# Kernel optimization log

Measured on AMD Instinct MI355X. Metric: run time of the kernel, lower is better.

Reference implementation:

```python
import jax, jax.numpy as jnp
import numpy as np
import math

EMBED = 1024
HEADS = 16
B, S = 2, 1024

def setup_inputs() -> dict:
    key = jax.random.key(0)
    ks = jax.random.split(key, 6)
    sc = 1.0 / math.sqrt(EMBED)
    return {
        "x": jax.random.normal(ks[0], (B, S, EMBED), dtype=jnp.float32),
        "Wq": jax.random.normal(ks[1], (EMBED, EMBED), dtype=jnp.float32) * sc,
        "Wk": jax.random.normal(ks[2], (EMBED, EMBED), dtype=jnp.float32) * sc,
        "Wv": jax.random.normal(ks[3], (EMBED, EMBED), dtype=jnp.float32) * sc,
        "Wo": jax.random.normal(ks[4], (EMBED, EMBED), dtype=jnp.float32) * sc,
        "bo": jax.random.normal(ks[5], (EMBED,), dtype=jnp.float32) * sc,
        "heads": HEADS,
    }

def reference(x, Wq, Wk, Wv, Wo, bo, heads):
    nB, nS, nE = x.shape
    nH = heads
    nG = nE // nH  # effective number of 'heads' in this (quirky) module

    def split(W):
        # (B,S,E) -> (B,S,G,H) -> (B,G,S,H); per-head dim is nH (as in source)
        return (x @ W).reshape(nB, nS, nG, nH).transpose(0, 2, 1, 3)

    q, k, v = split(Wq), split(Wk), split(Wv)
    # scale uses k.size(-1) == heads, matching the source
    att = jnp.einsum('bgsh,bgth->bgst', q, k) / math.sqrt(nH)
    causal = jnp.tril(jnp.ones((nS, nS), dtype=bool))  # True = keep
    att = jnp.where(causal, att, -jnp.inf)
    att = jax.nn.softmax(att, axis=-1)
    y = jnp.einsum('bgst,bgth->bgsh', att, v)
    y = y.transpose(0, 2, 1, 3).reshape(nB, nS, nE)
    return y @ Wo + bo
```

## Files before the change

kernel.cpp:

```cpp
#include <hip/hip_runtime.h>
#include <hip/hip_bf16.h>
#include <stdint.h>

typedef __attribute__((ext_vector_type(8))) short bf16x8;
typedef __attribute__((ext_vector_type(4))) short bf16x4;
typedef __attribute__((ext_vector_type(4))) float f32x4;

#define NB 2
#define SEQ 1024
#define EMB 1024
#define NH 16
#define NG 64

#if defined(__has_builtin)
#if __has_builtin(__builtin_amdgcn_mfma_f32_16x16x16bf16_1k)
#define QK_1K 1
#else
#define QK_1K 0
#endif
#if __has_builtin(__builtin_amdgcn_exp2f)
#define EXP2(x) __builtin_amdgcn_exp2f(x)
#else
#define EXP2(x) exp2f(x)
#endif
#if __has_builtin(__builtin_amdgcn_rcpf)
#define RCP(x) __builtin_amdgcn_rcpf(x)
#else
#define RCP(x) (1.0f / (x))
#endif
#else
#define QK_1K 0
#define EXP2(x) exp2f(x)
#define RCP(x) (1.0f / (x))
#endif

__device__ __forceinline__ unsigned short f2bf(float f){
  uint32_t u = __float_as_uint(f);
  uint32_t r = (u + 0x7fffu + ((u >> 16) & 1u)) >> 16;
  return (unsigned short)r;
}

__device__ __forceinline__ uint32_t pack_bf2(float lo, float hi){
  uint32_t a = (__float_as_uint(lo) + 0x8000u) >> 16;
  uint32_t b = (__float_as_uint(hi) + 0x8000u) & 0xffff0000u;
  return a | b;
}

__device__ __forceinline__ void gld_lds16(const void* g, void* l){
  __builtin_amdgcn_global_load_lds((__attribute__((address_space(1))) void*)(uintptr_t)(g),
                                   (__attribute__((address_space(3))) void*)(l),
                                   16, 0, 0);
}


__global__ __launch_bounds__(256) void prep_kernel(
    const float* __restrict__ x,
    const float* __restrict__ W0, const float* __restrict__ W1,
    const float* __restrict__ W2, const float* __restrict__ W3,
    unsigned short* __restrict__ xb,
    unsigned short* __restrict__ wtAll)
{
  const int bid = blockIdx.x;
  if (bid < 2048){
    int i = (bid * 256 + threadIdx.x) * 4;
    float4 f = *(const float4*)(x + i);
    ushort4 o;
    o.x = f2bf(f.x); o.y = f2bf(f.y); o.z = f2bf(f.z); o.w = f2bf(f.w);
    *(ushort4*)(xb + i) = o;
    return;
  }
  __shared__ float tile[32][33];
  const int b2 = bid - 2048;
  const int z = b2 & 3;
  const int rest = b2 >> 2;
  const float* W = (z == 0) ? W0 : (z == 1) ? W1 : (z == 2) ? W2 : W3;
  unsigned short* o = wtAll + (size_t)z * EMB * EMB;
  const int n0 = (rest & 31) * 32, k0 = (rest >> 5) * 32;
  const int tx = threadIdx.x & 31, ty = threadIdx.x >> 5;
#pragma unroll
  for (int i = 0; i < 4; i++)
    tile[ty + 8*i][tx] = W[(size_t)(k0 + ty + 8*i) * EMB + n0 + tx];
  __syncthreads();
#pragma unroll
  for (int i = 0; i < 4; i++)
    o[(size_t)(n0 + ty + 8*i) * EMB + k0 + tx] = f2bf(tile[tx][ty + 8*i]);
}


template<int J>
__device__ __forceinline__ void stage_tile(const unsigned short* __restrict__ src,
                                           unsigned short* __restrict__ dst,
                                           int row0, int k0, int t){
#pragma unroll
  for (int j = 0; j < J; ++j){
    const int c = t + 256 * j;
    const int row = c >> 3;
    const int col8 = (c & 7) ^ (row & 7);
    gld_lds16(src + (size_t)(row0 + row) * 1024 + k0 + col8 * 8, dst + c * 8);
  }
}


__global__ __launch_bounds__(256) void gemm_qkv_kernel(
    const unsigned short* __restrict__ A,
    const unsigned short* __restrict__ WtAll,
    unsigned short* __restrict__ qws,
    unsigned short* __restrict__ kws,
    unsigned short* __restrict__ vws)
{
  __shared__ unsigned short As[2][128][64];
  __shared__ unsigned short Bs[2][64][64];
  const int z = blockIdx.z;
  const unsigned short* Bp = WtAll + (size_t)z * EMB * EMB;
  const int m0 = blockIdx.x * 128, n0 = blockIdx.y * 64;
  const int t = threadIdx.x;
  const int l = t & 63, w = t >> 6;
  const int wr = w >> 1, wc = w & 1;
  const int lr = l & 15, lk = l >> 4;
  const int sw0 = (lk ^ (lr & 7)) * 8;
  const int sw1 = ((lk + 4) ^ (lr & 7)) * 8;

  f32x4 acc[4][2];
#pragma unroll
  for (int m = 0; m < 4; m++)
#pragma unroll
    for (int n = 0; n < 2; n++)
#pragma unroll
      for (int r = 0; r < 4; r++) acc[m][n][r] = 0.f;

  stage_tile<4>(A, &As[0][0][0], m0, 0, t);
  stage_tile<2>(Bp, &Bs[0][0][0], n0, 0, t);
  __syncthreads();
  int cur = 0;
  for (int kt = 0; kt < 16; ++kt){
    if (kt < 15){
      stage_tile<4>(A, &As[cur ^ 1][0][0], m0, (kt + 1) * 64, t);
      stage_tile<2>(Bp, &Bs[cur ^ 1][0][0], n0, (kt + 1) * 64, t);
    }
#pragma unroll
    for (int half = 0; half < 2; ++half){
      const int sw = half ? sw1 : sw0;
      bf16x8 af[4], bfr[2];
#pragma unroll
      for (int m = 0; m < 4; m++) af[m]  = *(const bf16x8*)(&As[cur][wr*64 + m*16 + lr][sw]);
#pragma unroll
      for (int n = 0; n < 2; n++) bfr[n] = *(const bf16x8*)(&Bs[cur][wc*32 + n*16 + lr][sw]);
#pragma unroll
      for (int m = 0; m < 4; m++)
#pragma unroll
        for (int n = 0; n < 2; n++)
          acc[m][n] = __builtin_amdgcn_mfma_f32_16x16x32_bf16(af[m], bfr[n], acc[m][n], 0, 0, 0);
    }
    __syncthreads();
    cur ^= 1;
  }

#pragma unroll
  for (int m = 0; m < 4; m++){
    const int rowb = m0 + wr*64 + m*16 + lk*4;
#pragma unroll
    for (int n = 0; n < 2; n++){
      const int col = n0 + wc*32 + n*16 + lr;
      const int g = col >> 4, h = col & 15;
#pragma unroll
      for (int r = 0; r < 4; r++){
        const int rr = rowb + r;
        const int b = rr >> 10, s = rr & 1023;
        const int bg = b * NG + g;
        const float v = acc[m][n][r];
        if (z == 0)      qws[((size_t)bg * 1024 + s) * 16 + h] = f2bf(v * 0.36067376022f);
        else if (z == 1) kws[((size_t)bg * 1024 + s) * 16 + h] = f2bf(v);
        else             vws[((size_t)bg * 16 + h) * 1024 + s] = f2bf(v);
      }
    }
  }
}


__global__ __launch_bounds__(256) void gemm_out_kernel(
    const unsigned short* __restrict__ A,
    const unsigned short* __restrict__ Bw,
    const float* __restrict__ bo,
    float* __restrict__ out)
{
  __shared__ unsigned short As[2][64][64];
  __shared__ unsigned short Bs[2][64][64];
  const int m0 = blockIdx.x * 64, n0 = blockIdx.y * 64;
  const int t = threadIdx.x;
  const int l = t & 63, w = t >> 6;
  const int wr = w >> 1, wc = w & 1;
  const int lr = l & 15, lk = l >> 4;
  const int sw0 = (lk ^ (lr & 7)) * 8;
  const int sw1 = ((lk + 4) ^ (lr & 7)) * 8;

  f32x4 acc[2][2];
#pragma unroll
  for (int m = 0; m < 2; m++)
#pragma unroll
    for (int n = 0; n < 2; n++)
#pragma unroll
      for (int r = 0; r < 4; r++) acc[m][n][r] = 0.f;

  stage_tile<2>(A, &As[0][0][0], m0, 0, t);
  stage_tile<2>(Bw, &Bs[0][0][0], n0, 0, t);
  __syncthreads();
  int cur = 0;
  for (int kt = 0; kt < 16; ++kt){
    if (kt < 15){
      stage_tile<2>(A, &As[cur ^ 1][0][0], m0, (kt + 1) * 64, t);
      stage_tile<2>(Bw, &Bs[cur ^ 1][0][0], n0, (kt + 1) * 64, t);
    }
#pragma unroll
    for (int half = 0; half < 2; ++half){
      const int sw = half ? sw1 : sw0;
      bf16x8 af[2], bfr[2];
#pragma unroll
      for (int m = 0; m < 2; m++) af[m]  = *(const bf16x8*)(&As[cur][wr*32 + m*16 + lr][sw]);
#pragma unroll
      for (int n = 0; n < 2; n++) bfr[n] = *(const bf16x8*)(&Bs[cur][wc*32 + n*16 + lr][sw]);
#pragma unroll
      for (int m = 0; m < 2; m++)
#pragma unroll
        for (int n = 0; n < 2; n++)
          acc[m][n] = __builtin_amdgcn_mfma_f32_16x16x32_bf16(af[m], bfr[n], acc[m][n], 0, 0, 0);
    }
    __syncthreads();
    cur ^= 1;
  }

#pragma unroll
  for (int m = 0; m < 2; m++){
    const int rowb = m0 + wr*32 + m*16 + lk*4;
#pragma unroll
    for (int n = 0; n < 2; n++){
      const int col = n0 + wc*32 + n*16 + lr;
      const float bb = bo[col];
#pragma unroll
      for (int r = 0; r < 4; r++)
        out[(size_t)(rowb + r) * 1024 + col] = acc[m][n][r] + bb;
    }
  }
}


#if QK_1K
struct KF { bf16x4 f[4]; };
#else
struct KF { bf16x8 f[4]; };
#endif

__device__ __forceinline__ void attn_tile(
#if QK_1K
    const bf16x4& aq,
#else
    const bf16x8& aq,
#endif
    const KF& kc, const bf16x8& bv0, const bf16x8& bv1,
    f32x4& yacc0, f32x4& yacc1, f32x4& sfr0, f32x4& sfr1,
    unsigned short (*pw)[72],
    int c0, int nt, int tt, int lr, int lk, const bf16x8& bone)
{
  const int t0 = tt << 6;
  f32x4 sacc[4];
#pragma unroll
  for (int ts = 0; ts < 4; ++ts){
    f32x4 zc;
#pragma unroll
    for (int r = 0; r < 4; r++) zc[r] = 0.f;
#if QK_1K
    sacc[ts] = __builtin_amdgcn_mfma_f32_16x16x16bf16_1k(kc.f[ts], aq, zc, 0, 0, 0);
#else
    sacc[ts] = __builtin_amdgcn_mfma_f32_16x16x32_bf16(kc.f[ts], aq, zc, 0, 0, 0);
#endif
  }

  if (tt == nt - 1){
    const int qrow = c0 + lr;
#pragma unroll
    for (int ts = 0; ts < 4; ++ts){
      const int key0 = t0 + ts*16 + lk*4;
#pragma unroll
      for (int r = 0; r < 4; ++r)
        if (key0 + r > qrow) sacc[ts][r] = -1e30f;
    }
  }

#pragma unroll
  for (int ts = 0; ts < 4; ++ts){
    const float e0 = EXP2(sacc[ts][0]);
    const float e1 = EXP2(sacc[ts][1]);
    const float e2 = EXP2(sacc[ts][2]);
    const float e3 = EXP2(sacc[ts][3]);
    uint2 u; u.x = pack_bf2(e0, e1); u.y = pack_bf2(e2, e3);
    *(uint2*)(&pw[lr][ts*16 + lk*4]) = u;
  }

  const bf16x8 ap0 = *(const bf16x8*)(&pw[lr][lk * 8]);
  const bf16x8 ap1 = *(const bf16x8*)(&pw[lr][32 + lk * 8]);

  sfr0  = __builtin_amdgcn_mfma_f32_16x16x32_bf16(ap0, bone,  sfr0, 0, 0, 0);
  sfr1  = __builtin_amdgcn_mfma_f32_16x16x32_bf16(ap1, bone,  sfr1, 0, 0, 0);
  yacc0 = __builtin_amdgcn_mfma_f32_16x16x32_bf16(ap0, bv0, yacc0, 0, 0, 0);
  yacc1 = __builtin_amdgcn_mfma_f32_16x16x32_bf16(ap1, bv1, yacc1, 0, 0, 0);
}

__global__ __launch_bounds__(256, 4) void attn_kernel(
    const unsigned short* __restrict__ q,
    const unsigned short* __restrict__ k,
    const unsigned short* __restrict__ vt,
    unsigned short* __restrict__ y)
{
  const int blk = blockIdx.x;
  const int bg = blk & 127;
  const int pg = blk >> 7;
  const int t = threadIdx.x, w = t >> 6, l = t & 63;
  const int lr = l & 15, lk = l >> 4;
  const int wvv = 31 - (pg * 4 + w);
  const int cA = 2 * wvv;
  const int c0A = cA * 16, c0B = c0A + 16;
  const int nt = (cA >> 2) + 1;

  __shared__ unsigned short p_lds[8][16][72];
  unsigned short (*pwA)[72] = p_lds[w * 2];
  unsigned short (*pwB)[72] = p_lds[w * 2 + 1];

  const unsigned short* qb = q + (size_t)bg * 1024 * 16;
  const unsigned short* kb = k + (size_t)bg * 1024 * 16;
  const unsigned short* vb = vt + (size_t)bg * 16 * 1024;
  const int b = bg >> 6, g = bg & 63;

  bf16x8 bone;
#pragma unroll
  for (int i = 0; i < 8; i++) bone[i] = (short)0x3F80;

#if QK_1K
  const bf16x4 aqA = *(const bf16x4*)(qb + (size_t)(c0A + lr) * 16 + lk * 4);
  const bf16x4 aqB = *(const bf16x4*)(qb + (size_t)(c0B + lr) * 16 + lk * 4);
#else
  bf16x8 aqA, aqB;
#pragma unroll
  for (int i = 0; i < 8; i++){ aqA[i] = 0; aqB[i] = 0; }
  if (lk < 2){
    aqA = *(const bf16x8*)(qb + (size_t)(c0A + lr) * 16 + lk * 8);
    aqB = *(const bf16x8*)(qb + (size_t)(c0B + lr) * 16 + lk * 8);
  }
#endif

  f32x4 yA0, yA1, sA0, sA1, yB0, yB1, sB0, sB1;
#pragma unroll
  for (int r = 0; r < 4; r++){
    yA0[r] = yA1[r] = sA0[r] = sA1[r] = 0.f;
    yB0[r] = yB1[r] = sB0[r] = sB1[r] = 0.f;
  }

  KF kc, kn;
#if !QK_1K
#pragma unroll
  for (int ts = 0; ts < 4; ++ts)
#pragma unroll
    for (int i = 0; i < 8; i++){ kc.f[ts][i] = 0; kn.f[ts][i] = 0; }
#endif
#pragma unroll
  for (int ts = 0; ts < 4; ++ts){
#if QK_1K
    kc.f[ts] = *(const bf16x4*)(kb + (size_t)(ts*16 + lr) * 16 + lk * 4);
#else
    if (lk < 2) kc.f[ts] = *(const bf16x8*)(kb + (size_t)(ts*16 + lr) * 16 + lk * 8);
#endif
  }

  for (int tt = 0; tt < nt; ++tt){
    const int t0 = tt << 6;

    if (tt + 1 < nt){
      const int t1 = t0 + 64;
#pragma unroll
      for (int ts = 0; ts < 4; ++ts){
#if QK_1K
        kn.f[ts] = *(const bf16x4*)(kb + (size_t)(t1 + ts*16 + lr) * 16 + lk * 4);
#else
        if (lk < 2) kn.f[ts] = *(const bf16x8*)(kb + (size_t)(t1 + ts*16 + lr) * 16 + lk * 8);
#endif
      }
    }
    const bf16x8 bv0 = *(const bf16x8*)(vb + (size_t)lr * 1024 + t0 + lk * 8);
    const bf16x8 bv1 = *(const bf16x8*)(vb + (size_t)lr * 1024 + t0 + 32 + lk * 8);

    attn_tile(aqA, kc, bv0, bv1, yA0, yA1, sA0, sA1, pwA, c0A, nt, tt, lr, lk, bone);
    attn_tile(aqB, kc, bv0, bv1, yB0, yB1, sB0, sB1, pwB, c0B, nt, tt, lr, lk, bone);

    kc = kn;
  }

#pragma unroll
  for (int r = 0; r < 4; ++r){
    const int sAi = c0A + lk*4 + r;
    const float vA = (yA0[r] + yA1[r]) * RCP(sA0[r] + sA1[r]);
    y[((size_t)b * 1024 + sAi) * 1024 + g * 16 + lr] = f2bf(vA);
    const int sBi = c0B + lk*4 + r;
    const float vB = (yB0[r] + yB1[r]) * RCP(sB0[r] + sB1[r]);
    y[((size_t)b * 1024 + sBi) * 1024 + g * 16 + lr] = f2bf(vB);
  }
}


extern "C" void kernel_launch(void* const* d_in, const int* in_sizes, int n_in,
                              void* d_out, int out_size, void* d_ws, size_t ws_size,
                              hipStream_t stream)
{
  const float* x  = (const float*)d_in[0];
  const float* Wq = (const float*)d_in[1];
  const float* Wk = (const float*)d_in[2];
  const float* Wv = (const float*)d_in[3];
  const float* Wo = (const float*)d_in[4];
  const float* bo = (const float*)d_in[5];
  float* out = (float*)d_out;
  char* ws = (char*)d_ws;

  unsigned short* xb  = (unsigned short*)(ws);
  unsigned short* wt  = (unsigned short*)(ws + (4u << 20));
  unsigned short* qws = (unsigned short*)(ws + (12u << 20));
  unsigned short* kws = (unsigned short*)(ws + (16u << 20));
  unsigned short* vws = (unsigned short*)(ws + (20u << 20));
  unsigned short* yws = (unsigned short*)(ws);

  prep_kernel<<<6144, 256, 0, stream>>>(x, Wq, Wk, Wv, Wo, xb, wt);
  gemm_qkv_kernel<<<dim3(16, 16, 3), 256, 0, stream>>>(xb, wt, qws, kws, vws);
  attn_kernel<<<1024, 256, 0, stream>>>(qws, kws, vws, yws);
  gemm_out_kernel<<<dim3(32, 16), 256, 0, stream>>>(yws, wt + (size_t)3 * 1024 * 1024, bo, out);
}
```

Measured before the change: 69.55 us.

## Fuse Q/K/V projections into one block sharing the staged A tile

The QKV GEMM now computes all three projections in each block: one 64x64 A tile of x is staged once and multiplied against three 64x64 weight tiles, instead of launching a separate z-slice per weight with a 128-row A tile. This cuts repeated global loads of x and changes the grid from 768 blocks to 512. In exchange each block keeps more accumulators (12 MFMA tiles per wave), uses more LDS for the three B buffers, and writes all three outputs in its epilogue, which may lower occupancy.

```diff
diff --git a/kernel.cpp b/kernel.cpp
--- a/kernel.cpp
+++ b/kernel.cpp
@@ -108,11 +108,12 @@
     unsigned short* __restrict__ kws,
     unsigned short* __restrict__ vws)
 {
-  __shared__ unsigned short As[2][128][64];
-  __shared__ unsigned short Bs[2][64][64];
-  const int z = blockIdx.z;
-  const unsigned short* Bp = WtAll + (size_t)z * EMB * EMB;
-  const int m0 = blockIdx.x * 128, n0 = blockIdx.y * 64;
+  __shared__ unsigned short As[2][64][64];
+  __shared__ unsigned short Bs[2][3][64][64];
+  const unsigned short* B0 = WtAll;
+  const unsigned short* B1 = WtAll + (size_t)EMB * EMB;
+  const unsigned short* B2 = WtAll + (size_t)2 * EMB * EMB;
+  const int m0 = blockIdx.x * 64, n0 = blockIdx.y * 64;
   const int t = threadIdx.x;
   const int l = t & 63, w = t >> 6;
   const int wr = w >> 1, wc = w & 1;
@@ -120,44 +121,57 @@
   const int sw0 = (lk ^ (lr & 7)) * 8;
   const int sw1 = ((lk + 4) ^ (lr & 7)) * 8;
 
-  f32x4 acc[4][2];
-#pragma unroll
-  for (int m = 0; m < 4; m++)
-#pragma unroll
-    for (int n = 0; n < 2; n++)
-#pragma unroll
-      for (int r = 0; r < 4; r++) acc[m][n][r] = 0.f;
-
-  stage_tile<4>(A, &As[0][0][0], m0, 0, t);
-  stage_tile<2>(Bp, &Bs[0][0][0], n0, 0, t);
+  f32x4 acc[3][2][2];
+#pragma unroll
+  for (int z = 0; z < 3; z++)
+#pragma unroll
+    for (int m = 0; m < 2; m++)
+#pragma unroll
+      for (int n = 0; n < 2; n++)
+#pragma unroll
+        for (int r = 0; r < 4; r++) acc[z][m][n][r] = 0.f;
+
+  stage_tile<2>(A,  &As[0][0][0],    m0, 0, t);
+  stage_tile<2>(B0, &Bs[0][0][0][0], n0, 0, t);
+  stage_tile<2>(B1, &Bs[0][1][0][0], n0, 0, t);
+  stage_tile<2>(B2, &Bs[0][2][0][0], n0, 0, t);
   __syncthreads();
   int cur = 0;
   for (int kt = 0; kt < 16; ++kt){
     if (kt < 15){
-      stage_tile<4>(A, &As[cur ^ 1][0][0], m0, (kt + 1) * 64, t);
-      stage_tile<2>(Bp, &Bs[cur ^ 1][0][0], n0, (kt + 1) * 64, t);
+      const int k1 = (kt + 1) * 64;
+      stage_tile<2>(A,  &As[cur^1][0][0],    m0, k1, t);
+      stage_tile<2>(B0, &Bs[cur^1][0][0][0], n0, k1, t);
+      stage_tile<2>(B1, &Bs[cur^1][1][0][0], n0, k1, t);
+      stage_tile<2>(B2, &Bs[cur^1][2][0][0], n0, k1, t);
     }
 #pragma unroll
     for (int half = 0; half < 2; ++half){
       const int sw = half ? sw1 : sw0;
-      bf16x8 af[4], bfr[2];
-#pragma unroll
-      for (int m = 0; m < 4; m++) af[m]  = *(const bf16x8*)(&As[cur][wr*64 + m*16 + lr][sw]);
-#pragma unroll
-      for (int n = 0; n < 2; n++) bfr[n] = *(const bf16x8*)(&Bs[cur][wc*32 + n*16 + lr][sw]);
-#pragma unroll
-      for (int m = 0; m < 4; m++)
+      bf16x8 af[2];
+#pragma unroll
+      for (int m = 0; m < 2; m++)
+        af[m] = *(const bf16x8*)(&As[cur][wr*32 + m*16 + lr][sw]);
+#pragma unroll
+      for (int z = 0; z < 3; z++){
+        bf16x8 bfr[2];
 #pragma unroll
         for (int n = 0; n < 2; n++)
-          acc[m][n] = __builtin_amdgcn_mfma_f32_16x16x32_bf16(af[m], bfr[n], acc[m][n], 0, 0, 0);
+          bfr[n] = *(const bf16x8*)(&Bs[cur][z][wc*32 + n*16 + lr][sw]);
+#pragma unroll
+        for (int m = 0; m < 2; m++)
+#pragma unroll
+          for (int n = 0; n < 2; n++)
+            acc[z][m][n] = __builtin_amdgcn_mfma_f32_16x16x32_bf16(af[m], bfr[n], acc[z][m][n], 0, 0, 0);
+      }
     }
     __syncthreads();
     cur ^= 1;
   }
 
 #pragma unroll
-  for (int m = 0; m < 4; m++){
-    const int rowb = m0 + wr*64 + m*16 + lk*4;
+  for (int m = 0; m < 2; m++){
+    const int rowb = m0 + wr*32 + m*16 + lk*4;
 #pragma unroll
     for (int n = 0; n < 2; n++){
       const int col = n0 + wc*32 + n*16 + lr;
@@ -167,10 +181,9 @@
         const int rr = rowb + r;
         const int b = rr >> 10, s = rr & 1023;
         const int bg = b * NG + g;
-        const float v = acc[m][n][r];
-        if (z == 0)      qws[((size_t)bg * 1024 + s) * 16 + h] = f2bf(v * 0.36067376022f);
-        else if (z == 1) kws[((size_t)bg * 1024 + s) * 16 + h] = f2bf(v);
-        else             vws[((size_t)bg * 16 + h) * 1024 + s] = f2bf(v);
+        qws[((size_t)bg * 1024 + s) * 16 + h] = f2bf(acc[0][m][n][r] * 0.36067376022f);
+        kws[((size_t)bg * 1024 + s) * 16 + h] = f2bf(acc[1][m][n][r]);
+        vws[((size_t)bg * 16 + h) * 1024 + s] = f2bf(acc[2][m][n][r]);
       }
     }
   }
@@ -425,7 +438,7 @@
   unsigned short* yws = (unsigned short*)(ws);
 
   prep_kernel<<<6144, 256, 0, stream>>>(x, Wq, Wk, Wv, Wo, xb, wt);
-  gemm_qkv_kernel<<<dim3(16, 16, 3), 256, 0, stream>>>(xb, wt, qws, kws, vws);
+  gemm_qkv_kernel<<<dim3(32, 16), 256, 0, stream>>>(xb, wt, qws, kws, vws);
   attn_kernel<<<1024, 256, 0, stream>>>(qws, kws, vws, yws);
   gemm_out_kernel<<<dim3(32, 16), 256, 0, stream>>>(yws, wt + (size_t)3 * 1024 * 1024, bo, out);
 }
```

Result: faster. 67.24 us (-3.3%).

## Use 128x128 K32 tiles for fused QKV GEMM with LDS-transposed V stores

Applied to the files above, without the earlier changes.

The QKV projection moves from a 128x64 tile with K=64 over a 3D grid to a 128x128 tile with K=32, treating the three weight matrices as one concatenated N dimension. Each wave now computes a 4x4 block of MFMAs, which raises register accumulators but improves operand reuse. The V output, which is stored transposed, is first staged through LDS so it can be written with coalesced 16-byte stores instead of scattered 2-byte writes. The tile can straddle the q/k/v boundary only at multiples of 1024, so z is uniform per block.

```diff
diff --git a/kernel.cpp b/kernel.cpp
--- a/kernel.cpp
+++ b/kernel.cpp
@@ -100,77 +100,120 @@
   }
 }
 
+template<int J>
+__device__ __forceinline__ void stage_tile_k32(const unsigned short* __restrict__ src,
+                                               unsigned short* __restrict__ dst,
+                                               int row0, int k0, int t){
+#pragma unroll
+  for (int j = 0; j < J; ++j){
+    const int c = t + 256 * j;
+    const int row = c >> 2;
+    const int col8 = (c & 3) ^ (row & 3);
+    gld_lds16(src + (size_t)(row0 + row) * 1024 + k0 + col8 * 8, dst + c * 8);
+  }
+}
+
 
 __global__ __launch_bounds__(256) void gemm_qkv_kernel(
     const unsigned short* __restrict__ A,
-    const unsigned short* __restrict__ WtAll,
+    const unsigned short* __restrict__ Bc,
     unsigned short* __restrict__ qws,
     unsigned short* __restrict__ kws,
     unsigned short* __restrict__ vws)
 {
-  __shared__ unsigned short As[2][128][64];
-  __shared__ unsigned short Bs[2][64][64];
-  const int z = blockIdx.z;
-  const unsigned short* Bp = WtAll + (size_t)z * EMB * EMB;
-  const int m0 = blockIdx.x * 128, n0 = blockIdx.y * 64;
+  __shared__ __align__(16) unsigned short As[2][128][32];
+  __shared__ __align__(16) unsigned short Bs[2][128][32];
+  const int m0 = blockIdx.x * 128, n0 = blockIdx.y * 128;
   const int t = threadIdx.x;
   const int l = t & 63, w = t >> 6;
   const int wr = w >> 1, wc = w & 1;
   const int lr = l & 15, lk = l >> 4;
-  const int sw0 = (lk ^ (lr & 7)) * 8;
-  const int sw1 = ((lk + 4) ^ (lr & 7)) * 8;
-
-  f32x4 acc[4][2];
+  const int sw = (lk ^ (lr & 3)) * 8;
+
+  f32x4 acc[4][4];
 #pragma unroll
   for (int m = 0; m < 4; m++)
 #pragma unroll
-    for (int n = 0; n < 2; n++)
+    for (int n = 0; n < 4; n++)
 #pragma unroll
       for (int r = 0; r < 4; r++) acc[m][n][r] = 0.f;
 
-  stage_tile<4>(A, &As[0][0][0], m0, 0, t);
-  stage_tile<2>(Bp, &Bs[0][0][0], n0, 0, t);
+  stage_tile_k32<2>(A,  &As[0][0][0], m0, 0, t);
+  stage_tile_k32<2>(Bc, &Bs[0][0][0], n0, 0, t);
   __syncthreads();
   int cur = 0;
-  for (int kt = 0; kt < 16; ++kt){
-    if (kt < 15){
-      stage_tile<4>(A, &As[cur ^ 1][0][0], m0, (kt + 1) * 64, t);
-      stage_tile<2>(Bp, &Bs[cur ^ 1][0][0], n0, (kt + 1) * 64, t);
-    }
-#pragma unroll
-    for (int half = 0; half < 2; ++half){
-      const int sw = half ? sw1 : sw0;
-      bf16x8 af[4], bfr[2];
-#pragma unroll
-      for (int m = 0; m < 4; m++) af[m]  = *(const bf16x8*)(&As[cur][wr*64 + m*16 + lr][sw]);
-#pragma unroll
-      for (int n = 0; n < 2; n++) bfr[n] = *(const bf16x8*)(&Bs[cur][wc*32 + n*16 + lr][sw]);
-#pragma unroll
-      for (int m = 0; m < 4; m++)
-#pragma unroll
-        for (int n = 0; n < 2; n++)
-          acc[m][n] = __builtin_amdgcn_mfma_f32_16x16x32_bf16(af[m], bfr[n], acc[m][n], 0, 0, 0);
-    }
+  for (int kt = 0; kt < 32; ++kt){
+    if (kt < 31){
+      const int k1 = (kt + 1) * 32;
+      stage_tile_k32<2>(A,  &As[cur ^ 1][0][0], m0, k1, t);
+      stage_tile_k32<2>(Bc, &Bs[cur ^ 1][0][0], n0, k1, t);
+    }
+    bf16x8 af[4], bfr[4];
+#pragma unroll
+    for (int m = 0; m < 4; m++) af[m]  = *(const bf16x8*)(&As[cur][wr*64 + m*16 + lr][sw]);
+#pragma unroll
+    for (int n = 0; n < 4; n++) bfr[n] = *(const bf16x8*)(&Bs[cur][wc*64 + n*16 + lr][sw]);
+#pragma unroll
+    for (int m = 0; m < 4; m++)
+#pragma unroll
+      for (int n = 0; n < 4; n++)
+        acc[m][n] = __builtin_amdgcn_mfma_f32_16x16x32_bf16(af[m], bfr[n], acc[m][n], 0, 0, 0);
     __syncthreads();
     cur ^= 1;
   }
 
-#pragma unroll
-  for (int m = 0; m < 4; m++){
-    const int rowb = m0 + wr*64 + m*16 + lk*4;
-#pragma unroll
-    for (int n = 0; n < 2; n++){
-      const int col = n0 + wc*32 + n*16 + lr;
-      const int g = col >> 4, h = col & 15;
-#pragma unroll
-      for (int r = 0; r < 4; r++){
-        const int rr = rowb + r;
-        const int b = rr >> 10, s = rr & 1023;
+  const int z = n0 >> 10;
+  const int zn = n0 & 1023;
+  const int b = m0 >> 10, s0 = m0 & 1023;
+
+  if (z < 2){
+    const float scale = (z == 0) ? 0.36067376022f : 1.0f;
+    unsigned short* dst = (z == 0) ? qws : kws;
+#pragma unroll
+    for (int m = 0; m < 4; m++){
+      const int rowb = m0 + wr*64 + m*16 + lk*4;
+#pragma unroll
+      for (int n = 0; n < 4; n++){
+        const int colw = zn + wc*64 + n*16 + lr;
+        const int g = colw >> 4, h = colw & 15;
+#pragma unroll
+        for (int r = 0; r < 4; r++){
+          const int rr = rowb + r;
+          const int bb = rr >> 10, s = rr & 1023;
+          const int bg = bb * NG + g;
+          dst[((size_t)bg * 1024 + s) * 16 + h] = f2bf(acc[m][n][r] * scale);
+        }
+      }
+    }
+  } else {
+    unsigned short (*vtile)[136] = (unsigned short (*)[136])(&As[0][0][0]);
+#pragma unroll
+    for (int p = 0; p < 2; ++p){
+      __syncthreads();
+      if (wc == p){
+#pragma unroll
+        for (int m = 0; m < 4; m++){
+          const int rl = wr*64 + m*16 + lk*4;
+#pragma unroll
+          for (int n = 0; n < 4; n++){
+            const int cl = n*16 + lr;
+            uint2 u;
+            u.x = pack_bf2(acc[m][n][0], acc[m][n][1]);
+            u.y = pack_bf2(acc[m][n][2], acc[m][n][3]);
+            *(uint2*)(&vtile[cl][rl]) = u;
+          }
+        }
+      }
+      __syncthreads();
+      {
+        const int cl = t & 63, seg = t >> 6;
+        const int colw = zn + p*64 + cl;
+        const int g = colw >> 4, h = colw & 15;
         const int bg = b * NG + g;
-        const float v = acc[m][n][r];
-        if (z == 0)      qws[((size_t)bg * 1024 + s) * 16 + h] = f2bf(v * 0.36067376022f);
-        else if (z == 1) kws[((size_t)bg * 1024 + s) * 16 + h] = f2bf(v);
-        else             vws[((size_t)bg * 16 + h) * 1024 + s] = f2bf(v);
+        const uint4* src = (const uint4*)(&vtile[cl][seg * 32]);
+        uint4 v0 = src[0], v1 = src[1], v2 = src[2], v3 = src[3];
+        uint4* dst = (uint4*)(vws + ((size_t)bg * 16 + h) * 1024 + s0 + seg * 32);
+        dst[0] = v0; dst[1] = v1; dst[2] = v2; dst[3] = v3;
       }
     }
   }
@@ -371,7 +414,6 @@
 
   for (int tt = 0; tt < nt; ++tt){
     const int t0 = tt << 6;
-
     if (tt + 1 < nt){
       const int t1 = t0 + 64;
 #pragma unroll
@@ -422,10 +464,9 @@
   unsigned short* qws = (unsigned short*)(ws + (12u << 20));
   unsigned short* kws = (unsigned short*)(ws + (16u << 20));
   unsigned short* vws = (unsigned short*)(ws + (20u << 20));
-  unsigned short* yws = (unsigned short*)(ws);
 
   prep_kernel<<<6144, 256, 0, stream>>>(x, Wq, Wk, Wv, Wo, xb, wt);
-  gemm_qkv_kernel<<<dim3(16, 16, 3), 256, 0, stream>>>(xb, wt, qws, kws, vws);
-  attn_kernel<<<1024, 256, 0, stream>>>(qws, kws, vws, yws);
-  gemm_out_kernel<<<dim3(32, 16), 256, 0, stream>>>(yws, wt + (size_t)3 * 1024 * 1024, bo, out);
-}
+  gemm_qkv_kernel<<<dim3(16, 24), 256, 0, stream>>>(xb, wt, qws, kws, vws);
+  attn_kernel<<<1024, 256, 0, stream>>>(qws, kws, vws, xb);
+  gemm_out_kernel<<<dim3(32, 16), 256, 0, stream>>>(xb, wt + (size_t)3 * EMB * EMB, bo, out);
+}
```

Measured after the change: 75.45 us. 8.5% more time.
